# Kernel tuning notes

Hardware: AMD Instinct MI355X
Metric: run time of the kernel (lower is better)

## Reference

```python
import jax, jax.numpy as jnp
import numpy as np

BATCH, SEQ, IN_DIM, OUT_DIM, N_STATE = 16, 4096, 64, 64, 512


def setup_inputs() -> dict:
    key = jax.random.key(0)
    k_x, k_a, k_b, k_c, k_d = jax.random.split(key, 5)
    x = jax.random.normal(k_x, (BATCH, SEQ, IN_DIM), dtype=jnp.float32)
    # Stable transition matrix: spectral-norm-ish scaling keeps h bounded over SEQ steps.
    A = jax.random.normal(k_a, (N_STATE, N_STATE), dtype=jnp.float32) * (0.9 / np.sqrt(N_STATE))
    B = jax.random.normal(k_b, (N_STATE, IN_DIM), dtype=jnp.float32) / np.sqrt(IN_DIM)
    C = jax.random.normal(k_c, (OUT_DIM, N_STATE), dtype=jnp.float32) / np.sqrt(N_STATE)
    D = jax.random.normal(k_d, (OUT_DIM, IN_DIM), dtype=jnp.float32) / np.sqrt(IN_DIM)
    return {"x": x, "A": A, "B": B, "C": C, "D": D}


def reference(x, A, B, C, D):
    """Linear SSM recurrence: h_t = A h_{t-1} + B x_t ; y_t = C h_t + D x_t.

    x: [batch, seq, in_dim] -> y: [batch, seq, out_dim]
    """
    batch = x.shape[0]
    n = A.shape[0]
    # Precompute input projections once (batched GEMMs outside the scan).
    bx = jnp.einsum("ni,bsi->sbn", B, x)   # [seq, batch, n_state]
    dx = jnp.einsum("oi,bsi->bso", D, x)   # [batch, seq, out_dim]

    def step(h, bx_t):
        # h: [batch, n_state]; bx_t: [batch, n_state]
        h_new = h @ A.T + bx_t
        return h_new, h_new

    h0 = jnp.zeros((batch, n), dtype=x.dtype)
    _, hs = jax.lax.scan(step, h0, bx)      # hs: [seq, batch, n_state]
    y = jnp.einsum("on,sbn->bso", C, hs) + dx
    return y
```

## Files before the change

kernel.cpp:

```cpp
#include <hip/hip_runtime.h>
#include <cstdint>
#include <cstddef>

#define BATCH 16
#define SEQ   4096
#define NS    512
#define TLAG  128
#define PADR  128
#define PS    (SEQ + PADR)
#define CTILE 128
#define XROWS (CTILE + TLAG - 1)
#define XSTR  72
#define BLK   32768

typedef unsigned short u16;
typedef unsigned int   u32;
typedef short bf16x8 __attribute__((ext_vector_type(8)));
typedef float f32x4  __attribute__((ext_vector_type(4)));

__device__ __forceinline__ u16 f2bf(float f) {
    u32 u = __builtin_bit_cast(u32, f);
    return (u16)((u + 0x7FFFu + ((u >> 16) & 1u)) >> 16);
}
__device__ __forceinline__ float bf2f(u16 h) {
    return __builtin_bit_cast(float, (u32)h << 16);
}

__global__ __launch_bounds__(256) void prep_all(const float* __restrict__ x,
                                                const float* __restrict__ A,
                                                const float* __restrict__ B,
                                                const float* __restrict__ C,
                                                u16* __restrict__ xbf,
                                                u16* __restrict__ Arm,
                                                u16* __restrict__ At,
                                                u16* __restrict__ Rt,
                                                u16* __restrict__ L)
{
    const int bid = blockIdx.x;
    if (bid < 4224) {
        const int id = bid * 256 + threadIdx.x;
        const int b   = id / (PS * 16);
        const int rem = id - b * (PS * 16);
        const int p   = rem >> 4;
        const int g   = id & 15;
        ushort4 o;
        if (p < PADR) {
            o.x = 0; o.y = 0; o.z = 0; o.w = 0;
        } else {
            const float4 v = *(const float4*)(x + ((size_t)b * SEQ + (p - PADR)) * 64 + g * 4);
            o.x = f2bf(v.x); o.y = f2bf(v.y); o.z = f2bf(v.z); o.w = f2bf(v.w);
        }
        *(ushort4*)(xbf + ((size_t)b * PS + p) * 64 + g * 4) = o;
    } else {
        const int id = (bid - 4224) * 256 + threadIdx.x;
        if (id < 262144) {
            const int c = id & 511;
            const u16 v = f2bf(A[id]);
            Arm[id] = v;
            At[(size_t)c * 512 + (id >> 9)] = v;
        } else if (id < 262144 + 32768) {
            const int i = id - 262144;
            Rt[(size_t)(i & 63) * 512 + (i >> 6)] = f2bf(B[i]);
        } else if (id < 262144 + 65536) {
            const int i = id - 262144 - 32768;
            L[i] = f2bf(C[i]);
        }
    }
}

__device__ __forceinline__ void gemm_tile(const u16* __restrict__ apM,
                                          const u16* __restrict__ bT, int n0,
                                          u16* __restrict__ oRM,
                                          u16* __restrict__ oT, int rowT,
                                          u16* __restrict__ lds)
{
    const int tid = threadIdx.x;
    const int w = tid >> 6, l = tid & 63;
    const int lr = l & 15, q8 = (l >> 4) * 8;

    const u16* ap  = apM + (size_t)(w * 16 + lr) * NS + q8;
    const u16* bp0 = bT  + (size_t)(n0 + lr) * NS + q8;

    f32x4 acc[4];
    const f32x4 zero = {0.f, 0.f, 0.f, 0.f};
    #pragma unroll
    for (int nt = 0; nt < 4; ++nt) acc[nt] = zero;

    #pragma unroll 4
    for (int ks = 0; ks < 16; ++ks) {
        const bf16x8 a = *(const bf16x8*)(ap + ks * 32);
        #pragma unroll
        for (int nt = 0; nt < 4; ++nt) {
            const bf16x8 bfr = *(const bf16x8*)(bp0 + (size_t)nt * 16 * NS + ks * 32);
            acc[nt] = __builtin_amdgcn_mfma_f32_16x16x32_bf16(a, bfr, acc[nt], 0, 0, 0);
        }
    }

    const int rr = (l >> 4) * 4;
    if (oT) {
        #pragma unroll
        for (int nt = 0; nt < 4; ++nt) {
            const int col = n0 + nt * 16 + lr;
            ushort4 pk;
            pk.x = f2bf(acc[nt][0]); pk.y = f2bf(acc[nt][1]);
            pk.z = f2bf(acc[nt][2]); pk.w = f2bf(acc[nt][3]);
            *(ushort4*)(oT + (size_t)col * NS + rowT + w * 16 + rr) = pk;
        }
    }
    if (oRM) {
        #pragma unroll
        for (int nt = 0; nt < 4; ++nt)
            #pragma unroll
            for (int r = 0; r < 4; ++r)
                lds[(w * 16 + rr + r) * 72 + nt * 16 + lr] = f2bf(acc[nt][r]);
        __syncthreads();
        const int r  = tid >> 2;
        const int c0 = (tid & 3) * 16;
        #pragma unroll
        for (int k = 0; k < 4; ++k) {
            const ushort4 q = *(const ushort4*)&lds[r * 72 + c0 + k * 4];
            *(ushort4*)(oRM + (size_t)r * NS + n0 + c0 + k * 4) = q;
        }
    }
}

__global__ __launch_bounds__(256, 1) void stage_kernel(const u16* __restrict__ expAp,
                                                       const u16* __restrict__ expBT,
                                                       u16* __restrict__ expOut,
                                                       const u16* __restrict__ sqIn,
                                                       const u16* __restrict__ sqInT,
                                                       u16* __restrict__ sqOutRM,
                                                       u16* __restrict__ sqOutT,
                                                       int E)
{
    __shared__ u16 lds[64 * 72];
    const int t = blockIdx.x;
    if (t < E) {
        const int j = t >> 3, n0 = (t & 7) * 64;
        gemm_tile(expAp + (size_t)j * BLK, expBT, n0,
                  expOut + (size_t)j * BLK, nullptr, 0, lds);
    } else {
        const int tt = t - E;
        const int mr = tt >> 3, n0 = (tt & 7) * 64;
        gemm_tile(sqIn + (size_t)mr * BLK, sqInT, n0,
                  sqOutRM + (size_t)mr * BLK, sqOutT, mr * 64, lds);
    }
}

__global__ __launch_bounds__(256, 1) void g_kernel(const u16* __restrict__ Rt,
                                                   const u16* __restrict__ L,
                                                   const float* __restrict__ D,
                                                   u16* __restrict__ Gsw)
{
    __shared__ u16 lds[64 * 72];
    const int m = blockIdx.x;
    const int q = m >> 4, r = m & 15;
    const u16* ap0 = Rt + (size_t)q * BLK;
    const u16* bT0 = L  + (size_t)r * BLK;

    const int tid = threadIdx.x;
    const int w = tid >> 6, l = tid & 63;
    const int lr = l & 15, q8 = (l >> 4) * 8;

    const u16* ap  = ap0 + (size_t)(w * 16 + lr) * NS + q8;
    const u16* bp0 = bT0 + (size_t)lr * NS + q8;

    f32x4 acc[4];
    const f32x4 zero = {0.f, 0.f, 0.f, 0.f};
    #pragma unroll
    for (int nt = 0; nt < 4; ++nt) acc[nt] = zero;

    #pragma unroll 4
    for (int ks = 0; ks < 16; ++ks) {
        const bf16x8 a = *(const bf16x8*)(ap + ks * 32);
        #pragma unroll
        for (int nt = 0; nt < 4; ++nt) {
            const bf16x8 bfr = *(const bf16x8*)(bp0 + (size_t)nt * 16 * NS + ks * 32);
            acc[nt] = __builtin_amdgcn_mfma_f32_16x16x32_bf16(a, bfr, acc[nt], 0, 0, 0);
        }
    }

    const int rr = (l >> 4) * 4;
    #pragma unroll
    for (int nt = 0; nt < 4; ++nt)
        #pragma unroll
        for (int rk = 0; rk < 4; ++rk)
            lds[(nt * 16 + lr) * 72 + (w * 16 + rr + rk)] = f2bf(acc[nt][rk]);
    __syncthreads();

    const int f = tid >> 6;
    #pragma unroll
    for (int f2 = 0; f2 < 8; f2 += 4) {
        const int fi = f2 + f;
        const int ks = fi >> 2, nt = fi & 3;
        const int o  = nt * 16 + (l & 15);
        const int i0 = ks * 32 + (l >> 4) * 8;
        u16 v[8];
        #pragma unroll
        for (int j = 0; j < 8; ++j) {
            u16 gv = lds[o * 72 + i0 + j];
            if (m == 0) gv = f2bf(bf2f(gv) + D[o * 64 + i0 + j]);
            v[j] = gv;
        }
        ushort4 p0; p0.x = v[0]; p0.y = v[1]; p0.z = v[2]; p0.w = v[3];
        ushort4 p1; p1.x = v[4]; p1.y = v[5]; p1.z = v[6]; p1.w = v[7];
        u16* dst = Gsw + ((size_t)(m * 8 + fi) * 64 + l) * 8;
        *(ushort4*)(dst + 0) = p0;
        *(ushort4*)(dst + 4) = p1;
    }
}

__global__ __launch_bounds__(256, 2) void conv_kernel(const u16* __restrict__ xbf,
                                                      const u16* __restrict__ gsw,
                                                      float* __restrict__ y)
{
    __shared__ u16 Xs[XROWS * XSTR];
    __shared__ uint4 Gs[2][1024];

    const int tid = threadIdx.x;
    const int b  = blockIdx.y;
    const int t0 = blockIdx.x * CTILE;

    {
        const int g = tid & 7;
        int r = tid >> 3;
        const u16* src = xbf + ((size_t)b * PS + t0 + 1) * 64 + g * 8;
        #pragma unroll
        for (int it = 0; it < 8; ++it, r += 32) {
            if (r < XROWS) {
                const uint4 v = *(const uint4*)(src + (size_t)r * 64);
                *(uint4*)&Xs[r * XSTR + g * 8] = v;
            }
        }
    }

    const uint4* gp4 = (const uint4*)gsw;
    uint4 st[4];
    #pragma unroll
    for (int j = 0; j < 4; ++j) st[j] = gp4[tid + j * 256];

    const int w    = tid >> 6;
    const int l    = tid & 63;
    const int lr   = l & 15;
    const int q8   = (l >> 4) * 8;
    const int wrow = w * 32;

    f32x4 acc[2][4];
    const f32x4 zero = {0.f, 0.f, 0.f, 0.f};
    #pragma unroll
    for (int mt = 0; mt < 2; ++mt)
        #pragma unroll
        for (int nt = 0; nt < 4; ++nt) acc[mt][nt] = zero;

    #pragma unroll
    for (int j = 0; j < 4; ++j) Gs[0][tid + j * 256] = st[j];
    __syncthreads();

    for (int p = 0; p < 64; ++p) {
        const int cur = p & 1;
        if (p < 63) {
            #pragma unroll
            for (int j = 0; j < 4; ++j) st[j] = gp4[(p + 1) * 1024 + tid + j * 256];
        }
        #pragma unroll
        for (int sub = 0; sub < 2; ++sub) {
            const int m = 2 * p + sub;
            bf16x8 bc[8];
            #pragma unroll
            for (int f = 0; f < 8; ++f)
                bc[f] = __builtin_bit_cast(bf16x8, Gs[cur][sub * 512 + f * 64 + l]);

            const int rbase = wrow + lr + (TLAG - 1) - m;
            bf16x8 a[2][2];
            #pragma unroll
            for (int mt = 0; mt < 2; ++mt)
                #pragma unroll
                for (int ks = 0; ks < 2; ++ks)
                    a[mt][ks] = *(const bf16x8*)&Xs[(rbase + mt * 16) * XSTR + ks * 32 + q8];

            #pragma unroll
            for (int ks = 0; ks < 2; ++ks)
                #pragma unroll
                for (int mt = 0; mt < 2; ++mt)
                    #pragma unroll
                    for (int nt = 0; nt < 4; ++nt)
                        acc[mt][nt] = __builtin_amdgcn_mfma_f32_16x16x32_bf16(
                            a[mt][ks], bc[ks * 4 + nt], acc[mt][nt], 0, 0, 0);
        }
        if (p < 63) {
            #pragma unroll
            for (int j = 0; j < 4; ++j) Gs[cur ^ 1][tid + j * 256] = st[j];
        }
        __syncthreads();
    }

    const int rr = (l >> 4) * 4;
    #pragma unroll
    for (int mt = 0; mt < 2; ++mt) {
        #pragma unroll
        for (int nt = 0; nt < 4; ++nt) {
            const int t = t0 + wrow + mt * 16 + rr;
            const int o = nt * 16 + lr;
            float* yp = y + ((size_t)b * SEQ + t) * 64 + o;
            #pragma unroll
            for (int r = 0; r < 4; ++r) yp[(size_t)r * 64] = acc[mt][nt][r];
        }
    }
}

extern "C" void kernel_launch(void* const* d_in, const int* in_sizes, int n_in,
                              void* d_out, int out_size, void* d_ws, size_t ws_size,
                              hipStream_t stream)
{
    const float* x = (const float*)d_in[0];
    const float* A = (const float*)d_in[1];
    const float* B = (const float*)d_in[2];
    const float* C = (const float*)d_in[3];
    const float* D = (const float*)d_in[4];
    float* y = (float*)d_out;

    char* w = (char*)d_ws;
    u16* xbf   = (u16*)(w + 0);
    u16* Arm   = (u16*)(w + 8650752);
    u16* At    = (u16*)(w + 9175040);
    u16* A2rm  = (u16*)(w + 9699328);
    u16* A2t   = (u16*)(w + 10223616);
    u16* A4rm  = (u16*)(w + 10747904);
    u16* A4t   = (u16*)(w + 11272192);
    u16* A8rm  = (u16*)(w + 11796480);
    u16* A8t   = (u16*)(w + 12320768);
    u16* A16rm = (u16*)(w + 12845056);
    u16* A16t  = (u16*)(w + 13369344);
    u16* A32rm = (u16*)(w + 13893632);
    u16* A32t  = (u16*)(w + 14417920);
    u16* A64rm = (u16*)(w + 14942208);
    u16* L     = (u16*)(w + 15532032);
    u16* Rt    = (u16*)(w + 16580608);
    u16* Gsw   = (u16*)(w + 17104896);

    prep_all<<<5504, 256, 0, stream>>>(x, A, B, C, xbf, Arm, At, Rt, L);

    stage_kernel<<<72, 256, 0, stream>>>(L, At, L + 1 * BLK,
                                         Arm, At, A2rm, A2t, 8);
    stage_kernel<<<80, 256, 0, stream>>>(L, A2t, L + 2 * BLK,
                                         A2rm, A2t, A4rm, A4t, 16);
    stage_kernel<<<96, 256, 0, stream>>>(L, A4t, L + 4 * BLK,
                                         A4rm, A4t, A8rm, A8t, 32);
    stage_kernel<<<128, 256, 0, stream>>>(L, A8t, L + 8 * BLK,
                                          A8rm, A8t, A16rm, A16t, 64);
    stage_kernel<<<72, 256, 0, stream>>>(Rt, A16rm, Rt + 1 * BLK,
                                         A16rm, A16t, A32rm, A32t, 8);
    stage_kernel<<<80, 256, 0, stream>>>(Rt, A32rm, Rt + 2 * BLK,
                                         A32rm, A32t, A64rm, nullptr, 16);
    stage_kernel<<<32, 256, 0, stream>>>(Rt, A64rm, Rt + 4 * BLK,
                                         nullptr, nullptr, nullptr, nullptr, 32);
    g_kernel<<<128, 256, 0, stream>>>(Rt, L, D, Gsw);

    conv_kernel<<<dim3(SEQ / CTILE, BATCH), 256, 0, stream>>>(xbf, Gsw, y);
}
```

Measured before the change: 235.3 us.

## Fuse x bf16 conversion into conv kernel and double conv tile size

Drops the separate padded bf16 copy of x and instead converts fp32 x to bf16 inside the conv kernel while filling shared memory, zero-filling negative time indices. This removes an 8.6MB write and re-read pass. The conv tile grows from 128 to 256 timesteps (each wave does 4 M-tiles) with occupancy lowered to 1 block per SM, halving the number of filter streams per output but giving only 256 blocks and more registers per thread.

Measured after the change: 255.8 us. +8.7%, slower.

```diff
diff --git a/kernel.cpp b/kernel.cpp
--- a/kernel.cpp
+++ b/kernel.cpp
@@ -6,9 +6,7 @@
 #define SEQ   4096
 #define NS    512
 #define TLAG  128
-#define PADR  128
-#define PS    (SEQ + PADR)
-#define CTILE 128
+#define CTILE 256
 #define XROWS (CTILE + TLAG - 1)
 #define XSTR  72
 #define BLK   32768
@@ -26,45 +24,26 @@
     return __builtin_bit_cast(float, (u32)h << 16);
 }
 
-__global__ __launch_bounds__(256) void prep_all(const float* __restrict__ x,
-                                                const float* __restrict__ A,
+__global__ __launch_bounds__(256) void prep_mat(const float* __restrict__ A,
                                                 const float* __restrict__ B,
                                                 const float* __restrict__ C,
-                                                u16* __restrict__ xbf,
                                                 u16* __restrict__ Arm,
                                                 u16* __restrict__ At,
                                                 u16* __restrict__ Rt,
                                                 u16* __restrict__ L)
 {
-    const int bid = blockIdx.x;
-    if (bid < 4224) {
-        const int id = bid * 256 + threadIdx.x;
-        const int b   = id / (PS * 16);
-        const int rem = id - b * (PS * 16);
-        const int p   = rem >> 4;
-        const int g   = id & 15;
-        ushort4 o;
-        if (p < PADR) {
-            o.x = 0; o.y = 0; o.z = 0; o.w = 0;
-        } else {
-            const float4 v = *(const float4*)(x + ((size_t)b * SEQ + (p - PADR)) * 64 + g * 4);
-            o.x = f2bf(v.x); o.y = f2bf(v.y); o.z = f2bf(v.z); o.w = f2bf(v.w);
-        }
-        *(ushort4*)(xbf + ((size_t)b * PS + p) * 64 + g * 4) = o;
+    const int id = blockIdx.x * 256 + threadIdx.x;
+    if (id < 262144) {
+        const int c = id & 511;
+        const u16 v = f2bf(A[id]);
+        Arm[id] = v;
+        At[(size_t)c * 512 + (id >> 9)] = v;
+    } else if (id < 262144 + 32768) {
+        const int i = id - 262144;
+        Rt[(size_t)(i & 63) * 512 + (i >> 6)] = f2bf(B[i]);
     } else {
-        const int id = (bid - 4224) * 256 + threadIdx.x;
-        if (id < 262144) {
-            const int c = id & 511;
-            const u16 v = f2bf(A[id]);
-            Arm[id] = v;
-            At[(size_t)c * 512 + (id >> 9)] = v;
-        } else if (id < 262144 + 32768) {
-            const int i = id - 262144;
-            Rt[(size_t)(i & 63) * 512 + (i >> 6)] = f2bf(B[i]);
-        } else if (id < 262144 + 65536) {
-            const int i = id - 262144 - 32768;
-            L[i] = f2bf(C[i]);
-        }
+        const int i = id - 262144 - 32768;
+        L[i] = f2bf(C[i]);
     }
 }
 
@@ -210,7 +189,7 @@
     }
 }
 
-__global__ __launch_bounds__(256, 2) void conv_kernel(const u16* __restrict__ xbf,
+__global__ __launch_bounds__(256, 1) void conv_kernel(const float* __restrict__ x,
                                                       const u16* __restrict__ gsw,
                                                       float* __restrict__ y)
 {
@@ -222,14 +201,20 @@
     const int t0 = blockIdx.x * CTILE;
 
     {
-        const int g = tid & 7;
-        int r = tid >> 3;
-        const u16* src = xbf + ((size_t)b * PS + t0 + 1) * 64 + g * 8;
-        #pragma unroll
-        for (int it = 0; it < 8; ++it, r += 32) {
+        const int g = tid & 15;
+        int r = tid >> 4;
+        #pragma unroll
+        for (int it = 0; it < 24; ++it, r += 16) {
             if (r < XROWS) {
-                const uint4 v = *(const uint4*)(src + (size_t)r * 64);
-                *(uint4*)&Xs[r * XSTR + g * 8] = v;
+                const int t = t0 + r - (TLAG - 1);
+                ushort4 o;
+                if (t < 0) {
+                    o.x = 0; o.y = 0; o.z = 0; o.w = 0;
+                } else {
+                    const float4 v = *(const float4*)(x + ((size_t)b * SEQ + t) * 64 + g * 4);
+                    o.x = f2bf(v.x); o.y = f2bf(v.y); o.z = f2bf(v.z); o.w = f2bf(v.w);
+                }
+                *(ushort4*)&Xs[r * XSTR + g * 4] = o;
             }
         }
     }
@@ -243,12 +228,12 @@
     const int l    = tid & 63;
     const int lr   = l & 15;
     const int q8   = (l >> 4) * 8;
-    const int wrow = w * 32;
-
-    f32x4 acc[2][4];
+    const int wrow = w * 64;
+
+    f32x4 acc[4][4];
     const f32x4 zero = {0.f, 0.f, 0.f, 0.f};
     #pragma unroll
-    for (int mt = 0; mt < 2; ++mt)
+    for (int mt = 0; mt < 4; ++mt)
         #pragma unroll
         for (int nt = 0; nt < 4; ++nt) acc[mt][nt] = zero;
 
@@ -271,9 +256,9 @@
                 bc[f] = __builtin_bit_cast(bf16x8, Gs[cur][sub * 512 + f * 64 + l]);
 
             const int rbase = wrow + lr + (TLAG - 1) - m;
-            bf16x8 a[2][2];
-            #pragma unroll
-            for (int mt = 0; mt < 2; ++mt)
+            bf16x8 a[4][2];
+            #pragma unroll
+            for (int mt = 0; mt < 4; ++mt)
                 #pragma unroll
                 for (int ks = 0; ks < 2; ++ks)
                     a[mt][ks] = *(const bf16x8*)&Xs[(rbase + mt * 16) * XSTR + ks * 32 + q8];
@@ -281,7 +266,7 @@
             #pragma unroll
             for (int ks = 0; ks < 2; ++ks)
                 #pragma unroll
-                for (int mt = 0; mt < 2; ++mt)
+                for (int mt = 0; mt < 4; ++mt)
                     #pragma unroll
                     for (int nt = 0; nt < 4; ++nt)
                         acc[mt][nt] = __builtin_amdgcn_mfma_f32_16x16x32_bf16(
@@ -296,7 +281,7 @@
 
     const int rr = (l >> 4) * 4;
     #pragma unroll
-    for (int mt = 0; mt < 2; ++mt) {
+    for (int mt = 0; mt < 4; ++mt) {
         #pragma unroll
         for (int nt = 0; nt < 4; ++nt) {
             const int t = t0 + wrow + mt * 16 + rr;
@@ -320,7 +305,6 @@
     float* y = (float*)d_out;
 
     char* w = (char*)d_ws;
-    u16* xbf   = (u16*)(w + 0);
     u16* Arm   = (u16*)(w + 8650752);
     u16* At    = (u16*)(w + 9175040);
     u16* A2rm  = (u16*)(w + 9699328);
@@ -338,7 +322,7 @@
     u16* Rt    = (u16*)(w + 16580608);
     u16* Gsw   = (u16*)(w + 17104896);
 
-    prep_all<<<5504, 256, 0, stream>>>(x, A, B, C, xbf, Arm, At, Rt, L);
+    prep_mat<<<1280, 256, 0, stream>>>(A, B, C, Arm, At, Rt, L);
 
     stage_kernel<<<72, 256, 0, stream>>>(L, At, L + 1 * BLK,
                                          Arm, At, A2rm, A2t, 8);
@@ -356,5 +340,5 @@
                                          nullptr, nullptr, nullptr, nullptr, 32);
     g_kernel<<<128, 256, 0, stream>>>(Rt, L, D, Gsw);
 
-    conv_kernel<<<dim3(SEQ / CTILE, BATCH), 256, 0, stream>>>(xbf, Gsw, y);
-}
+    conv_kernel<<<dim3(SEQ / CTILE, BATCH), 256, 0, stream>>>(x, Gsw, y);
+}
```
